# Performance work log

Measured on AMD Instinct MI355X. Metric: run time of the kernel, lower is better.

The kernel has to match this reference:

```python
import jax, jax.numpy as jnp
import numpy as np

DIM = 256
HEADS = 8
H = 32
W = 32
N = H * W  # must equal 4*DIM for the BatchNorm1d(dim*4) over the token dim to be valid
TAU = 2.0
V_TH = 1.0


def _rope_rotations():
    # RoPE buffer: shape (H, W, DIM//2) angles; k_max = DIM // (2*2)
    k_max = DIM // 4
    theta = 1.0 / (10000.0 ** (jnp.arange(k_max, dtype=jnp.float32) / k_max))
    hg, wg = jnp.meshgrid(jnp.arange(H, dtype=jnp.float32), jnp.arange(W, dtype=jnp.float32), indexing='ij')
    angles = jnp.concatenate([hg[..., None] * theta, wg[..., None] * theta], axis=-1)  # (H,W,DIM//2)
    return jnp.cos(angles), jnp.sin(angles)


def _apply_rope(x, cos, sin):
    # x: (b,H,W,DIM); complex rotation on consecutive (re,im) pairs
    x2 = x.reshape(*x.shape[:-1], -1, 2)
    re, im = x2[..., 0], x2[..., 1]
    out = jnp.stack([cos * re - sin * im, sin * re + cos * im], axis=-1)
    return out.reshape(x.shape)


def _lif(x):
    # MultiStepLIFNode(tau=2.0, detach_reset=True): time axis = axis 0 (here batch, as in source),
    # decay_input=True, v_reset=0 (hard reset), heaviside fwd + sigmoid(alpha=4) surrogate bwd.
    def step(v, xt):
        v = v + (xt - v) / TAU
        sg = jax.nn.sigmoid(4.0 * (v - V_TH))
        spike = jax.lax.stop_gradient((v >= V_TH).astype(x.dtype) - sg) + sg
        v = v * (1.0 - jax.lax.stop_gradient(spike))  # detach_reset hard reset to 0
        return v, spike
    _, s = jax.lax.scan(step, jnp.zeros_like(x[0]), x)
    return s


def setup_inputs() -> dict:
    key = jax.random.key(0)
    ks = jax.random.split(key, 4)
    x = jax.random.normal(ks[0], (8, N, DIM), dtype=jnp.float32)
    Wqk = jax.random.normal(ks[1], (DIM, 2 * DIM), dtype=jnp.float32) * 0.02
    bqk = jnp.zeros((2 * DIM,), dtype=jnp.float32)
    bn_gamma = jnp.ones((N,), dtype=jnp.float32)
    bn_beta = jnp.zeros((N,), dtype=jnp.float32)
    lepe_w = jax.random.normal(ks[2], (DIM, 1, 3, 3), dtype=jnp.float32) * 0.1
    lepe_b = jnp.zeros((DIM,), dtype=jnp.float32)
    return {"x": x, "Wqk": Wqk, "bqk": bqk, "bn_gamma": bn_gamma, "bn_beta": bn_beta,
            "lepe_w": lepe_w, "lepe_b": lepe_b}


def reference(x, Wqk, bqk, bn_gamma, bn_beta, lepe_w, lepe_b):
    b, n, c = x.shape
    hd = c // HEADS
    cos, sin = _rope_rotations()

    qk = x @ Wqk + bqk  # (b,n,2c)
    # Dropout is identity in eval. BatchNorm1d(4*dim) in eval mode: channels = token dim (n == 4*dim),
    # running_mean=0, running_var=1 -> pure affine per token index.
    qk = qk * bn_gamma[None, :, None] + bn_beta[None, :, None]
    qk = _lif(qk)
    q, k = qk[..., :c], qk[..., c:]  # reshape(b,n,2,c) split
    v = x
    q = jax.nn.elu(q) + 1.0
    k = jax.nn.elu(k) + 1.0

    q_rope = _apply_rope(q.reshape(b, H, W, c), cos, sin).reshape(b, n, HEADS, hd).transpose(0, 2, 1, 3)
    k_rope = _apply_rope(k.reshape(b, H, W, c), cos, sin).reshape(b, n, HEADS, hd).transpose(0, 2, 1, 3)
    qh = q.reshape(b, n, HEADS, hd).transpose(0, 2, 1, 3)  # (b,h,n,d)
    kh = k.reshape(b, n, HEADS, hd).transpose(0, 2, 1, 3)
    vh = v.reshape(b, n, HEADS, hd).transpose(0, 2, 1, 3)

    atten = jnp.einsum('bhnd,bhmd->bhnm', qh, kh)  # returned, not used for output
    kmean = kh.mean(axis=2, keepdims=True)  # (b,h,1,d)
    z = 1.0 / (jnp.einsum('bhnd,bhed->bhne', qh, kmean) + 1e-6)  # (b,h,n,1)
    kv = jnp.einsum('bhnd,bhne->bhde', k_rope, vh) / n  # (k^T n^-0.5) @ (v n^-0.5)
    out = jnp.einsum('bhnd,bhde->bhne', q_rope, kv) * z  # (b,h,n,d)
    out = out.transpose(0, 2, 1, 3).reshape(b, n, c)

    v_img = vh.transpose(0, 2, 1, 3).reshape(b, H, W, c).transpose(0, 3, 1, 2)  # (b,c,H,W)
    lepe = jax.lax.conv_general_dilated(v_img, lepe_w, (1, 1), 'SAME',
                                        feature_group_count=c,
                                        dimension_numbers=('NCHW', 'OIHW', 'NCHW'))
    lepe = lepe + lepe_b[None, :, None, None]
    out = out + lepe.transpose(0, 2, 3, 1).reshape(b, n, c)
    return (out, qh, kh, v_img, atten)
```

## Files before the change

### kernel.cpp

```cpp
#include <hip/hip_runtime.h>
#include <cstdint>
#include <cstddef>

#define OFF_OUT   0
#define OFF_QH    2097152
#define OFF_KH    4194304
#define OFF_VIMG  6291456
#define OFF_ATT   8388608

#define WS_MQ   0
#define WS_MK   65536
#define WS_TBL  131072
#define WS_KVP  393216
#define WS_KMP  655360

typedef float f32x4 __attribute__((ext_vector_type(4)));

__device__ __forceinline__ void gemm_lif_512(
    const float* __restrict__ x, const float* __restrict__ Wqk,
    const float* __restrict__ bqk, const float* __restrict__ gamma,
    const float* __restrict__ beta, unsigned* __restrict__ mq,
    unsigned* __restrict__ mk, float* smem, unsigned* nib,
    int blk_n, int blk_c, int t)
{
    int ks = t >> 8, tl = t & 255;
    int n0 = blk_n * 8, c0 = blk_c * 128;
    int c_t = tl & 31, n_l = tl >> 5;
    float* xs  = smem + ks * 2176;
    float* wsb = smem + 4352 + ks * 4224;

    float acc[8][4];
    #pragma unroll
    for (int b = 0; b < 8; ++b)
        #pragma unroll
        for (int j = 0; j < 4; ++j) acc[b][j] = 0.f;

    int um = tl >> 3, ukq = tl & 7;
    const float* gx1 = x + ((size_t)(um & 7) * 1024 + n0 + (um >> 3)) * 256 + ks * 128 + ukq * 4;
    const float* gx2 = gx1 + 4 * 256;
    float* lx1 = xs + (ukq * 4) * 68 + um;
    float* lx2 = lx1 + 32;
    const float* gw = Wqk + ((size_t)ks * 128 + (tl >> 5)) * 512 + c0 + (tl & 31) * 4;
    float* lw0 = wsb + (tl >> 5) * 132 + (tl & 31) * 4;

    f32x4 px0, px1, pw0, pw1, pw2, pw3;
    px0 = *(const f32x4*)(gx1);
    px1 = *(const f32x4*)(gx2);
    pw0 = *(const f32x4*)(gw);
    pw1 = *(const f32x4*)(gw + 8 * 512);
    pw2 = *(const f32x4*)(gw + 16 * 512);
    pw3 = *(const f32x4*)(gw + 24 * 512);

    for (int p = 0; p < 4; ++p) {
        #pragma unroll
        for (int j = 0; j < 4; ++j) { lx1[j * 68] = px0[j]; lx2[j * 68] = px1[j]; }
        *(f32x4*)(lw0)            = pw0;
        *(f32x4*)(lw0 + 8 * 132)  = pw1;
        *(f32x4*)(lw0 + 16 * 132) = pw2;
        *(f32x4*)(lw0 + 24 * 132) = pw3;
        __syncthreads();
        if (p < 3) {
            int ko = (p + 1) * 32;
            px0 = *(const f32x4*)(gx1 + ko);
            px1 = *(const f32x4*)(gx2 + ko);
            pw0 = *(const f32x4*)(gw + (ko + 0) * 512);
            pw1 = *(const f32x4*)(gw + (ko + 8) * 512);
            pw2 = *(const f32x4*)(gw + (ko + 16) * 512);
            pw3 = *(const f32x4*)(gw + (ko + 24) * 512);
        }
        #pragma unroll 8
        for (int kk = 0; kk < 32; ++kk) {
            f32x4 xa  = *(const f32x4*)(xs + kk * 68 + n_l * 8);
            f32x4 xb2 = *(const f32x4*)(xs + kk * 68 + n_l * 8 + 4);
            f32x4 w4  = *(const f32x4*)(wsb + kk * 132 + c_t * 4);
            #pragma unroll
            for (int b = 0; b < 4; ++b)
                #pragma unroll
                for (int j = 0; j < 4; ++j)
                    acc[b][j] = fmaf(xa[b], w4[j], acc[b][j]);
            #pragma unroll
            for (int b = 0; b < 4; ++b)
                #pragma unroll
                for (int j = 0; j < 4; ++j)
                    acc[b + 4][j] = fmaf(xb2[b], w4[j], acc[b + 4][j]);
        }
        __syncthreads();
    }

    float* comb = smem;
    if (ks == 1) {
        #pragma unroll
        for (int idx = 0; idx < 32; ++idx)
            comb[idx * 257 + tl] = acc[idx >> 2][idx & 3];
    }
    __syncthreads();
    if (ks == 0) {
        #pragma unroll
        for (int idx = 0; idx < 32; ++idx)
            acc[idx >> 2][idx & 3] += comb[idx * 257 + tl];
        float g = gamma[n0 + n_l], be = beta[n0 + n_l];
        f32x4 bq = *(const f32x4*)&bqk[c0 + c_t * 4];
        float v0 = 0.f, v1 = 0.f, v2 = 0.f, v3 = 0.f;
        #pragma unroll
        for (int b = 0; b < 8; ++b) {
            float a0 = (acc[b][0] + bq[0]) * g + be;
            float a1 = (acc[b][1] + bq[1]) * g + be;
            float a2 = (acc[b][2] + bq[2]) * g + be;
            float a3 = (acc[b][3] + bq[3]) * g + be;
            v0 = v0 + (a0 - v0) * 0.5f; v1 = v1 + (a1 - v1) * 0.5f;
            v2 = v2 + (a2 - v2) * 0.5f; v3 = v3 + (a3 - v3) * 0.5f;
            unsigned s0 = (v0 >= 1.f), s1 = (v1 >= 1.f), s2 = (v2 >= 1.f), s3 = (v3 >= 1.f);
            v0 = s0 ? 0.f : v0; v1 = s1 ? 0.f : v1;
            v2 = s2 ? 0.f : v2; v3 = s3 ? 0.f : v3;
            nib[n_l * 256 + (c_t >> 3) * 64 + (c_t & 7) * 8 + b] =
                s0 | (s1 << 1) | (s2 << 2) | (s3 << 3);
        }
    }
    __syncthreads();
    if (t < 256) {
        int b = t & 7, hp = (t >> 3) & 3, nl = t >> 5;
        unsigned wd = 0;
        #pragma unroll
        for (int c8 = 0; c8 < 8; ++c8)
            wd |= nib[nl * 256 + hp * 64 + c8 * 8 + b] << (4 * c8);
        unsigned h = (unsigned)((blk_c & 1) * 4 + hp);
        unsigned* dst = (blk_c < 2) ? mq : mk;
        dst[b * 8192 + h * 1024 + n0 + nl] = wd;
    }
}

__global__ __launch_bounds__(512) void phaseA_kernel(
    const float* __restrict__ x, const float* __restrict__ Wqk,
    const float* __restrict__ bqk, const float* __restrict__ gamma,
    const float* __restrict__ beta, unsigned* __restrict__ mq,
    unsigned* __restrict__ mk, float* __restrict__ vimg,
    float* __restrict__ tbl)
{
    __shared__ float smem[12800];
    __shared__ unsigned nib[2048];
    int t = threadIdx.x;
    int blk = blockIdx.x;
    if (blk < 256) {
        gemm_lif_512(x, Wqk, bqk, gamma, beta, mq, mk, smem, nib,
                     blk >> 1, 2 + (blk & 1), t);
        return;
    }
    if (blk >= 1280) {
        int id = (blk - 1280) * 512 + t;
        int j = id & 127, n = id >> 7;
        int i = (j < 64) ? j : j - 64;
        float th = powf(10000.0f, -(float)i * (1.0f / 64.0f));
        float pos = (float)((j < 64) ? (n >> 5) : (n & 31));
        float ang = pos * th;
        tbl[n * 256 + j * 2]     = cosf(ang);
        tbl[n * 256 + j * 2 + 1] = sinf(ang);
        return;
    }
    int tile = (blk - 256) * 2 + (t >> 8);
    int st = t & 255;
    float* s = smem + (t >> 8) * 1056;
    int b = tile >> 8, ti = tile & 255;
    int p0 = (ti >> 3) * 32, c0 = (ti & 7) * 32;
    int row = st >> 3, c4 = (st & 7) * 4;
    const float4 vl = *(const float4*)&x[(b * 1024 + p0 + row) * 256 + c0 + c4];
    s[row * 33 + c4 + 0] = vl.x; s[row * 33 + c4 + 1] = vl.y;
    s[row * 33 + c4 + 2] = vl.z; s[row * 33 + c4 + 3] = vl.w;
    __syncthreads();
    int cc = st >> 3, p4 = (st & 7) * 4;
    f32x4 o;
    o.x = s[(p4 + 0) * 33 + cc]; o.y = s[(p4 + 1) * 33 + cc];
    o.z = s[(p4 + 2) * 33 + cc]; o.w = s[(p4 + 3) * 33 + cc];
    *(f32x4*)&vimg[(b * 256 + c0 + cc) * 1024 + p0 + p4] = o;
}

__global__ __launch_bounds__(512) void phaseB_kernel(
    const float* __restrict__ x, const float* __restrict__ Wqk,
    const float* __restrict__ bqk, const float* __restrict__ gamma,
    const float* __restrict__ beta, unsigned* __restrict__ mq,
    unsigned* __restrict__ mk, const float* __restrict__ tbl,
    float* __restrict__ kvp, float* __restrict__ kmp)
{
    __shared__ float smem[12800];
    __shared__ unsigned nib[2048];
    int t = threadIdx.x;
    int blk = blockIdx.x;
    if (blk < 256) {
        gemm_lif_512(x, Wqk, bqk, gamma, beta, mq, mk, smem, nib,
                     blk >> 1, blk & 1, t);
        return;
    }
    int ks2 = t >> 8, tl = t & 255;
    int unit = (blk - 256) * 2 + ks2;
    int bh = unit >> 2, seg = unit & 3;
    int b = bh >> 3, h = bh & 7;
    int n0 = seg * 256;
    float* kr   = smem + ks2 * 4800;
    float* vhs  = kr + 2304;
    float* part = kr + 4416;
    int d = tl & 31, ch = tl >> 5;
    int sc = 0;
    for (int i = 0; i < 32; ++i)
        sc += (mk[bh * 1024 + n0 + ch * 32 + i] >> d) & 1u;
    part[ch * 32 + d] = (float)sc;
    __syncthreads();
    if (tl < 32) {
        float cs = 0.f;
        #pragma unroll
        for (int j = 0; j < 8; ++j) cs += part[j * 32 + tl];
        kmp[bh * 128 + seg * 32 + tl] = cs;
    }
    float a0 = 0, a1 = 0, a2 = 0, a3 = 0;
    int e = tl & 31, db = (tl >> 5) * 4;
    for (int c0 = n0; c0 < n0 + 256; c0 += 64) {
        __syncthreads();
        #pragma unroll
        for (int i = 0; i < 8; ++i) {
            int f = tl + i * 256;
            int nn = f >> 5, dd = f & 31;
            int n = c0 + nn;
            unsigned w = mk[bh * 1024 + n];
            float kd = 1.0f + (float)((w >> dd) & 1u);
            float ko = 1.0f + (float)((w >> (dd ^ 1)) & 1u);
            const float* cp = tbl + n * 256 + h * 32 + (dd & ~1);
            float cc2 = cp[0], ss2 = cp[1];
            kr[nn * 36 + dd] = (dd & 1) ? (ss2 * ko + cc2 * kd) : (cc2 * kd - ss2 * ko);
            vhs[nn * 33 + dd] = x[(b * 1024 + n) * 256 + h * 32 + dd];
        }
        __syncthreads();
        #pragma unroll 8
        for (int nn = 0; nn < 64; ++nn) {
            float ve = vhs[nn * 33 + e];
            float4 kk = *(const float4*)&kr[nn * 36 + db];
            a0 = fmaf(kk.x, ve, a0); a1 = fmaf(kk.y, ve, a1);
            a2 = fmaf(kk.z, ve, a2); a3 = fmaf(kk.w, ve, a3);
        }
    }
    float* dst = kvp + bh * 4096 + seg * 1024;
    dst[(db + 0) * 32 + e] = a0;
    dst[(db + 1) * 32 + e] = a1;
    dst[(db + 2) * 32 + e] = a2;
    dst[(db + 3) * 32 + e] = a3;
}

__global__ __launch_bounds__(256) void phaseC_kernel(
    const unsigned* __restrict__ mq, const unsigned* __restrict__ mk,
    const float* __restrict__ x, const float* __restrict__ tbl,
    const float* __restrict__ kvp, const float* __restrict__ kmp,
    const float* __restrict__ lw, const float* __restrict__ lb,
    float* __restrict__ outbase)
{
    int t = threadIdx.x;
    if (blockIdx.x >= 512) {
        int blk = blockIdx.x - 512;
        int bh = blk >> 5;
        int tile = blk & 31;
        float* qh = outbase + OFF_QH;
        float* kh = outbase + OFF_KH;
        float* att = outbase + OFF_ATT;
        {
            int row = tile * 32 + (t >> 3);
            int d0 = (t & 7) * 4;
            unsigned wq = mq[bh * 1024 + row], wk = mk[bh * 1024 + row];
            f32x4 a, bb;
            a.x = 1.f + (float)((wq >> (d0 + 0)) & 1u);
            a.y = 1.f + (float)((wq >> (d0 + 1)) & 1u);
            a.z = 1.f + (float)((wq >> (d0 + 2)) & 1u);
            a.w = 1.f + (float)((wq >> (d0 + 3)) & 1u);
            bb.x = 1.f + (float)((wk >> (d0 + 0)) & 1u);
            bb.y = 1.f + (float)((wk >> (d0 + 1)) & 1u);
            bb.z = 1.f + (float)((wk >> (d0 + 2)) & 1u);
            bb.w = 1.f + (float)((wk >> (d0 + 3)) & 1u);
            *(f32x4*)&qh[((bh * 1024 + row) << 5) + d0] = a;
            *(f32x4*)&kh[((bh * 1024 + row) << 5) + d0] = bb;
        }
        uint4 mm = ((const uint4*)(mk + bh * 1024))[t];
        float4 rr;
        rr.x = (float)__popc(mm.x); rr.y = (float)__popc(mm.y);
        rr.z = (float)__popc(mm.z); rr.w = (float)__popc(mm.w);
        float* base = att + ((size_t)bh * 1024 + (size_t)tile * 32) * 1024;
        const unsigned* mqrow = mq + bh * 1024 + tile * 32;
        for (int row = 0; row < 32; ++row) {
            unsigned mqw = mqrow[row];
            float rq = 32.0f + (float)__popc(mqw);
            f32x4 o;
            o.x = rq + rr.x + (float)__popc(mqw & mm.x);
            o.y = rq + rr.y + (float)__popc(mqw & mm.y);
            o.z = rq + rr.z + (float)__popc(mqw & mm.z);
            o.w = rq + rr.w + (float)__popc(mqw & mm.w);
            ((f32x4*)(base + (size_t)row * 1024))[t] = o;
        }
        return;
    }
    int bi = blockIdx.x;
    int bh = bi >> 3, sub = bi & 7;
    int pseg = sub >> 1, half = sub & 1;
    int b = bh >> 3, h = bh & 7;
    bool hy = (h < 4);
    int e = t & 31, p_l = t >> 5;
    int p = pseg * 8 + p_l;
    int q0 = half * 16;
    float* out = outbase + OFF_OUT;

    __shared__ float kvs[32][32];
    __shared__ float kmf[32];
    __shared__ float zs[128];
    const float inv = 1.0f / 1024.0f;
    #pragma unroll
    for (int i = 0; i < 4; ++i) {
        int f = t + i * 256;
        const float* kp = kvp + bh * 4096 + f;
        kvs[f >> 5][f & 31] = (kp[0] + kp[1024] + kp[2048] + kp[3072]) * inv;
    }
    if (t < 32) {
        const float* mp = kmp + bh * 128 + t;
        kmf[t] = 1.0f + (mp[0] + mp[32] + mp[64] + mp[96]) * inv;
    }
    __syncthreads();
    float S = 0.f;
    #pragma unroll
    for (int dd = 0; dd < 32; ++dd) S += kmf[dd];
    if (t < 128) {
        int pl2 = t >> 4, iq = t & 15;
        int pp = pseg * 8 + pl2, qq = q0 + iq;
        int n = hy ? (pp * 32 + qq) : (qq * 32 + pp);
        unsigned w = mq[bh * 1024 + n];
        float acc = S;
        #pragma unroll
        for (int dd = 0; dd < 32; ++dd)
            acc += (float)((w >> dd) & 1u) * kmf[dd];
        zs[t] = 1.0f / (acc + 1e-6f);
    }
    int n_ref = hy ? (p * 32) : p;
    const float* cp = tbl + n_ref * 256 + h * 32;
    float E[16], O[16], B = 0.f;
    #pragma unroll
    for (int j = 0; j < 16; ++j) {
        float c2 = cp[2 * j], s2 = cp[2 * j + 1];
        float K0 = kvs[2 * j][e], K1 = kvs[2 * j + 1][e];
        E[j] = c2 * K0 + s2 * K1;
        O[j] = c2 * K1 - s2 * K0;
        B += E[j] + O[j];
    }
    __syncthreads();
    int c = h * 32 + e;
    float w9[9];
    #pragma unroll
    for (int j = 0; j < 9; ++j) w9[j] = lw[c * 9 + j];
    float lbv = lb[c];
    const float* xb = x + (size_t)b * 262144 + c;
    auto ld = [&](int yy, int xx) -> float {
        if ((unsigned)yy > 31u || (unsigned)xx > 31u) return 0.f;
        return xb[(yy * 32 + xx) * 256];
    };
    if (hy) {
        int y = p;
        float Wm0 = ld(y - 1, q0 - 1), Wm1 = ld(y, q0 - 1), Wm2 = ld(y + 1, q0 - 1);
        float Wc0 = ld(y - 1, q0),     Wc1 = ld(y, q0),     Wc2 = ld(y + 1, q0);
        #pragma unroll 4
        for (int i = 0; i < 16; ++i) {
            int m = q0 + i;
            float Wp0 = ld(y - 1, m + 1), Wp1 = ld(y, m + 1), Wp2 = ld(y + 1, m + 1);
            int n = y * 32 + m;
            unsigned w = mq[bh * 1024 + n];
            float o = B;
            #pragma unroll
            for (int j = 0; j < 16; ++j) {
                o += (float)((w >> (2 * j)) & 1u) * E[j];
                o += (float)((w >> (2 * j + 1)) & 1u) * O[j];
            }
            o *= zs[p_l * 16 + i];
            float l = lbv;
            l = fmaf(w9[0], Wm0, l); l = fmaf(w9[1], Wc0, l); l = fmaf(w9[2], Wp0, l);
            l = fmaf(w9[3], Wm1, l); l = fmaf(w9[4], Wc1, l); l = fmaf(w9[5], Wp1, l);
            l = fmaf(w9[6], Wm2, l); l = fmaf(w9[7], Wc2, l); l = fmaf(w9[8], Wp2, l);
            out[((b * 1024 + n) << 8) + c] = o + l;
            Wm0 = Wc0; Wm1 = Wc1; Wm2 = Wc2;
            Wc0 = Wp0; Wc1 = Wp1; Wc2 = Wp2;
        }
    } else {
        int xx0 = p;
        float Wm0 = ld(q0 - 1, xx0 - 1), Wm1 = ld(q0 - 1, xx0), Wm2 = ld(q0 - 1, xx0 + 1);
        float Wc0 = ld(q0, xx0 - 1),     Wc1 = ld(q0, xx0),     Wc2 = ld(q0, xx0 + 1);
        #pragma unroll 4
        for (int i = 0; i < 16; ++i) {
            int m = q0 + i;
            float Wp0 = ld(m + 1, xx0 - 1), Wp1 = ld(m + 1, xx0), Wp2 = ld(m + 1, xx0 + 1);
            int n = m * 32 + xx0;
            unsigned w = mq[bh * 1024 + n];
            float o = B;
            #pragma unroll
            for (int j = 0; j < 16; ++j) {
                o += (float)((w >> (2 * j)) & 1u) * E[j];
                o += (float)((w >> (2 * j + 1)) & 1u) * O[j];
            }
            o *= zs[p_l * 16 + i];
            float l = lbv;
            l = fmaf(w9[0], Wm0, l); l = fmaf(w9[1], Wm1, l); l = fmaf(w9[2], Wm2, l);
            l = fmaf(w9[3], Wc0, l); l = fmaf(w9[4], Wc1, l); l = fmaf(w9[5], Wc2, l);
            l = fmaf(w9[6], Wp0, l); l = fmaf(w9[7], Wp1, l); l = fmaf(w9[8], Wp2, l);
            out[((b * 1024 + n) << 8) + c] = o + l;
            Wm0 = Wc0; Wm1 = Wc1; Wm2 = Wc2;
            Wc0 = Wp0; Wc1 = Wp1; Wc2 = Wp2;
        }
    }
}

extern "C" void kernel_launch(void* const* d_in, const int* in_sizes, int n_in,
                              void* d_out, int out_size, void* d_ws, size_t ws_size,
                              hipStream_t stream)
{
    const float* x     = (const float*)d_in[0];
    const float* Wqk   = (const float*)d_in[1];
    const float* bqk   = (const float*)d_in[2];
    const float* gamma = (const float*)d_in[3];
    const float* beta  = (const float*)d_in[4];
    const float* lw    = (const float*)d_in[5];
    const float* lb    = (const float*)d_in[6];
    float* out = (float*)d_out;
    unsigned* ws = (unsigned*)d_ws;
    unsigned* mq = ws + WS_MQ;
    unsigned* mk = ws + WS_MK;
    float* tbl  = (float*)(ws + WS_TBL);
    float* kvp  = (float*)(ws + WS_KVP);
    float* kmp  = (float*)(ws + WS_KMP);

    hipLaunchKernelGGL(phaseA_kernel, dim3(1536), dim3(512), 0, stream,
                       x, Wqk, bqk, gamma, beta, mq, mk, out + OFF_VIMG, tbl);
    hipLaunchKernelGGL(phaseB_kernel, dim3(384), dim3(512), 0, stream,
                       x, Wqk, bqk, gamma, beta, mq, mk, tbl, kvp, kmp);
    hipLaunchKernelGGL(phaseC_kernel, dim3(2560), dim3(256), 0, stream,
                       mq, mk, x, tbl, kvp, kmp, lw, lb, out);
}
```

Measured before the change: 95.35 us.

## Restructure QK GEMM+LIF tile: per-wave token rows, double buffering, ballot spike packing

Rewrites the fused QK projection + LIF block so each wave owns one token row across all 8 timesteps and each lane computes two channels, replacing the split-K over two 256-thread halves and its shared-memory reduction. Weight and x tiles are double-buffered in LDS with one barrier per K step. Spike bits are packed with wave ballots and bit-spreading instead of going through a nibble scratch array and a second pass. This drops the cross-half reduction and extra syncs, at the cost of less register blocking per thread (16 accumulators instead of 32), which lowers FMA-to-load intensity.

```diff
diff --git a/kernel.cpp b/kernel.cpp
--- a/kernel.cpp
+++ b/kernel.cpp
@@ -16,116 +16,100 @@
 
 typedef float f32x4 __attribute__((ext_vector_type(4)));
 
+__device__ __forceinline__ unsigned spread2(unsigned v) {
+    v = (v | (v << 8)) & 0x00FF00FFu;
+    v = (v | (v << 4)) & 0x0F0F0F0Fu;
+    v = (v | (v << 2)) & 0x33333333u;
+    v = (v | (v << 1)) & 0x55555555u;
+    return v;
+}
+
 __device__ __forceinline__ void gemm_lif_512(
     const float* __restrict__ x, const float* __restrict__ Wqk,
     const float* __restrict__ bqk, const float* __restrict__ gamma,
     const float* __restrict__ beta, unsigned* __restrict__ mq,
-    unsigned* __restrict__ mk, float* smem, unsigned* nib,
+    unsigned* __restrict__ mk, float* pool,
     int blk_n, int blk_c, int t)
 {
-    int ks = t >> 8, tl = t & 255;
-    int n0 = blk_n * 8, c0 = blk_c * 128;
-    int c_t = tl & 31, n_l = tl >> 5;
-    float* xs  = smem + ks * 2176;
-    float* wsb = smem + 4352 + ks * 4224;
-
-    float acc[8][4];
-    #pragma unroll
-    for (int b = 0; b < 8; ++b)
+    const int w = t >> 6, lane = t & 63;
+    const int n0 = blk_n * 8, c0 = blk_c * 128;
+    const int n = n0 + w;
+    const float* gw = Wqk + (size_t)(t >> 5) * 512 + c0 + (t & 31) * 4;
+    const float* gx = x + ((size_t)(lane >> 3) * 1024 + n) * 256 + (lane & 7) * 4;
+    float* wd_base = pool + (t >> 5) * 128 + (t & 31) * 4;
+    float* xs_w    = pool + 8192 + w * 288 + (lane >> 3) * 36 + (lane & 7) * 4;
+    const float* xs_rd = pool + 8192 + w * 288;
+
+    float acc[8][2];
+    #pragma unroll
+    for (int b = 0; b < 8; ++b) { acc[b][0] = 0.f; acc[b][1] = 0.f; }
+
+    {
+        f32x4 wA = *(const f32x4*)(gw);
+        f32x4 wB = *(const f32x4*)(gw + (size_t)16 * 512);
+        f32x4 xr = *(const f32x4*)(gx);
+        *(f32x4*)(wd_base) = wA;
+        *(f32x4*)(wd_base + 2048) = wB;
+        *(f32x4*)(xs_w) = xr;
+    }
+    f32x4 wA_n = *(const f32x4*)(gw + (size_t)32 * 512);
+    f32x4 wB_n = *(const f32x4*)(gw + (size_t)48 * 512);
+    f32x4 xr_n = *(const f32x4*)(gx + 32);
+
+    for (int p = 0; p < 8; ++p) {
+        __syncthreads();
+        if (p < 7) {
+            int nb = (p + 1) & 1;
+            *(f32x4*)(wd_base + nb * 4096)        = wA_n;
+            *(f32x4*)(wd_base + nb * 4096 + 2048) = wB_n;
+            *(f32x4*)(xs_w + nb * 2304)           = xr_n;
+            if (p < 6) {
+                int ko = (p + 2) * 32;
+                wA_n = *(const f32x4*)(gw + (size_t)ko * 512);
+                wB_n = *(const f32x4*)(gw + (size_t)(ko + 16) * 512);
+                xr_n = *(const f32x4*)(gx + ko);
+            }
+        }
+        const float* wsp = pool + (p & 1) * 4096;
+        const float* xsp = xs_rd + (p & 1) * 2304;
         #pragma unroll
-        for (int j = 0; j < 4; ++j) acc[b][j] = 0.f;
-
-    int um = tl >> 3, ukq = tl & 7;
-    const float* gx1 = x + ((size_t)(um & 7) * 1024 + n0 + (um >> 3)) * 256 + ks * 128 + ukq * 4;
-    const float* gx2 = gx1 + 4 * 256;
-    float* lx1 = xs + (ukq * 4) * 68 + um;
-    float* lx2 = lx1 + 32;
-    const float* gw = Wqk + ((size_t)ks * 128 + (tl >> 5)) * 512 + c0 + (tl & 31) * 4;
-    float* lw0 = wsb + (tl >> 5) * 132 + (tl & 31) * 4;
-
-    f32x4 px0, px1, pw0, pw1, pw2, pw3;
-    px0 = *(const f32x4*)(gx1);
-    px1 = *(const f32x4*)(gx2);
-    pw0 = *(const f32x4*)(gw);
-    pw1 = *(const f32x4*)(gw + 8 * 512);
-    pw2 = *(const f32x4*)(gw + 16 * 512);
-    pw3 = *(const f32x4*)(gw + 24 * 512);
-
-    for (int p = 0; p < 4; ++p) {
-        #pragma unroll
-        for (int j = 0; j < 4; ++j) { lx1[j * 68] = px0[j]; lx2[j * 68] = px1[j]; }
-        *(f32x4*)(lw0)            = pw0;
-        *(f32x4*)(lw0 + 8 * 132)  = pw1;
-        *(f32x4*)(lw0 + 16 * 132) = pw2;
-        *(f32x4*)(lw0 + 24 * 132) = pw3;
-        __syncthreads();
-        if (p < 3) {
-            int ko = (p + 1) * 32;
-            px0 = *(const f32x4*)(gx1 + ko);
-            px1 = *(const f32x4*)(gx2 + ko);
-            pw0 = *(const f32x4*)(gw + (ko + 0) * 512);
-            pw1 = *(const f32x4*)(gw + (ko + 8) * 512);
-            pw2 = *(const f32x4*)(gw + (ko + 16) * 512);
-            pw3 = *(const f32x4*)(gw + (ko + 24) * 512);
-        }
-        #pragma unroll 8
-        for (int kk = 0; kk < 32; ++kk) {
-            f32x4 xa  = *(const f32x4*)(xs + kk * 68 + n_l * 8);
-            f32x4 xb2 = *(const f32x4*)(xs + kk * 68 + n_l * 8 + 4);
-            f32x4 w4  = *(const f32x4*)(wsb + kk * 132 + c_t * 4);
+        for (int kk4 = 0; kk4 < 8; ++kk4) {
+            f32x4 xv[8];
             #pragma unroll
-            for (int b = 0; b < 4; ++b)
+            for (int b = 0; b < 8; ++b)
+                xv[b] = *(const f32x4*)(xsp + b * 36 + kk4 * 4);
+            #pragma unroll
+            for (int j = 0; j < 4; ++j) {
+                float2 w2 = *(const float2*)(wsp + (kk4 * 4 + j) * 128 + lane * 2);
                 #pragma unroll
-                for (int j = 0; j < 4; ++j)
-                    acc[b][j] = fmaf(xa[b], w4[j], acc[b][j]);
-            #pragma unroll
-            for (int b = 0; b < 4; ++b)
-                #pragma unroll
-                for (int j = 0; j < 4; ++j)
-                    acc[b + 4][j] = fmaf(xb2[b], w4[j], acc[b + 4][j]);
-        }
-        __syncthreads();
-    }
-
-    float* comb = smem;
-    if (ks == 1) {
-        #pragma unroll
-        for (int idx = 0; idx < 32; ++idx)
-            comb[idx * 257 + tl] = acc[idx >> 2][idx & 3];
-    }
-    __syncthreads();
-    if (ks == 0) {
-        #pragma unroll
-        for (int idx = 0; idx < 32; ++idx)
-            acc[idx >> 2][idx & 3] += comb[idx * 257 + tl];
-        float g = gamma[n0 + n_l], be = beta[n0 + n_l];
-        f32x4 bq = *(const f32x4*)&bqk[c0 + c_t * 4];
-        float v0 = 0.f, v1 = 0.f, v2 = 0.f, v3 = 0.f;
-        #pragma unroll
-        for (int b = 0; b < 8; ++b) {
-            float a0 = (acc[b][0] + bq[0]) * g + be;
-            float a1 = (acc[b][1] + bq[1]) * g + be;
-            float a2 = (acc[b][2] + bq[2]) * g + be;
-            float a3 = (acc[b][3] + bq[3]) * g + be;
-            v0 = v0 + (a0 - v0) * 0.5f; v1 = v1 + (a1 - v1) * 0.5f;
-            v2 = v2 + (a2 - v2) * 0.5f; v3 = v3 + (a3 - v3) * 0.5f;
-            unsigned s0 = (v0 >= 1.f), s1 = (v1 >= 1.f), s2 = (v2 >= 1.f), s3 = (v3 >= 1.f);
-            v0 = s0 ? 0.f : v0; v1 = s1 ? 0.f : v1;
-            v2 = s2 ? 0.f : v2; v3 = s3 ? 0.f : v3;
-            nib[n_l * 256 + (c_t >> 3) * 64 + (c_t & 7) * 8 + b] =
-                s0 | (s1 << 1) | (s2 << 2) | (s3 << 3);
-        }
-    }
-    __syncthreads();
-    if (t < 256) {
-        int b = t & 7, hp = (t >> 3) & 3, nl = t >> 5;
-        unsigned wd = 0;
-        #pragma unroll
-        for (int c8 = 0; c8 < 8; ++c8)
-            wd |= nib[nl * 256 + hp * 64 + c8 * 8 + b] << (4 * c8);
-        unsigned h = (unsigned)((blk_c & 1) * 4 + hp);
-        unsigned* dst = (blk_c < 2) ? mq : mk;
-        dst[b * 8192 + h * 1024 + n0 + nl] = wd;
+                for (int b = 0; b < 8; ++b) {
+                    acc[b][0] = fmaf(xv[b][j], w2.x, acc[b][0]);
+                    acc[b][1] = fmaf(xv[b][j], w2.y, acc[b][1]);
+                }
+            }
+        }
+    }
+
+    float g = gamma[n], be = beta[n];
+    float2 bq = *(const float2*)&bqk[c0 + lane * 2];
+    unsigned* dst = (blk_c < 2) ? mq : mk;
+    int hbase = (blk_c & 1) * 4;
+    float v0 = 0.f, v1 = 0.f;
+    #pragma unroll
+    for (int b = 0; b < 8; ++b) {
+        float a0 = (acc[b][0] + bq.x) * g + be;
+        float a1 = (acc[b][1] + bq.y) * g + be;
+        v0 = v0 + (a0 - v0) * 0.5f;
+        v1 = v1 + (a1 - v1) * 0.5f;
+        bool s0 = (v0 >= 1.f), s1 = (v1 >= 1.f);
+        v0 = s0 ? 0.f : v0; v1 = s1 ? 0.f : v1;
+        unsigned long long m0 = __ballot(s0 ? 1 : 0);
+        unsigned long long m1 = __ballot(s1 ? 1 : 0);
+        if (lane < 4) {
+            unsigned a = (unsigned)(m0 >> (lane * 16)) & 0xFFFFu;
+            unsigned c = (unsigned)(m1 >> (lane * 16)) & 0xFFFFu;
+            dst[b * 8192 + (hbase + lane) * 1024 + n] = spread2(a) | (spread2(c) << 1);
+        }
     }
 }
 
@@ -137,11 +121,10 @@
     float* __restrict__ tbl)
 {
     __shared__ float smem[12800];
-    __shared__ unsigned nib[2048];
     int t = threadIdx.x;
     int blk = blockIdx.x;
     if (blk < 256) {
-        gemm_lif_512(x, Wqk, bqk, gamma, beta, mq, mk, smem, nib,
+        gemm_lif_512(x, Wqk, bqk, gamma, beta, mq, mk, smem,
                      blk >> 1, 2 + (blk & 1), t);
         return;
     }
@@ -181,11 +164,10 @@
     float* __restrict__ kvp, float* __restrict__ kmp)
 {
     __shared__ float smem[12800];
-    __shared__ unsigned nib[2048];
     int t = threadIdx.x;
     int blk = blockIdx.x;
     if (blk < 256) {
-        gemm_lif_512(x, Wqk, bqk, gamma, beta, mq, mk, smem, nib,
+        gemm_lif_512(x, Wqk, bqk, gamma, beta, mq, mk, smem,
                      blk >> 1, blk & 1, t);
         return;
     }
```

Measured after the change: 160.1 us. 1.68x slower.

## Shrink GEMM-LIF blocks to 256 threads with 8x8 register tiles

Applied to the files above, without the earlier changes.

The fused QK GEMM plus LIF routine now runs with 256 threads per block instead of 512, and each thread computes an 8x8 accumulator tile instead of 8x4. The W shared-memory layout is padded and interleaved to reduce bank conflicts, and spike bits are packed as bytes rather than nibbles. The auxiliary transpose, RoPE-table and kv-partial work in phases A and B is also re-split to one unit per 256-thread block. The aim is more register-level reuse per shared-memory load and finer-grained blocks, at the cost of higher register pressure and fewer threads per GEMM tile.

```diff
diff --git a/kernel.cpp b/kernel.cpp
--- a/kernel.cpp
+++ b/kernel.cpp
@@ -16,137 +16,149 @@
 
 typedef float f32x4 __attribute__((ext_vector_type(4)));
 
-__device__ __forceinline__ void gemm_lif_512(
+__device__ __forceinline__ int wcol(int g) { return g * 8 + 4 * (g >> 2); }
+
+__device__ __forceinline__ void gemm_lif_256(
     const float* __restrict__ x, const float* __restrict__ Wqk,
     const float* __restrict__ bqk, const float* __restrict__ gamma,
     const float* __restrict__ beta, unsigned* __restrict__ mq,
-    unsigned* __restrict__ mk, float* smem, unsigned* nib,
+    unsigned* __restrict__ mk, float* pool,
     int blk_n, int blk_c, int t)
 {
-    int ks = t >> 8, tl = t & 255;
-    int n0 = blk_n * 8, c0 = blk_c * 128;
-    int c_t = tl & 31, n_l = tl >> 5;
-    float* xs  = smem + ks * 2176;
-    float* wsb = smem + 4352 + ks * 4224;
-
-    float acc[8][4];
+    const int ks = t >> 7, tl = t & 127;
+    const int c_t = tl & 15, n_l = tl >> 4;
+    const int n0 = blk_n * 8, c0 = blk_c * 128;
+    float* wpool = pool + ks * 4480;
+    float* xpool = pool + 8960 + ks * 2176;
+
+    float acc[8][8];
     #pragma unroll
     for (int b = 0; b < 8; ++b)
         #pragma unroll
-        for (int j = 0; j < 4; ++j) acc[b][j] = 0.f;
-
-    int um = tl >> 3, ukq = tl & 7;
-    const float* gx1 = x + ((size_t)(um & 7) * 1024 + n0 + (um >> 3)) * 256 + ks * 128 + ukq * 4;
-    const float* gx2 = gx1 + 4 * 256;
-    float* lx1 = xs + (ukq * 4) * 68 + um;
-    float* lx2 = lx1 + 32;
-    const float* gw = Wqk + ((size_t)ks * 128 + (tl >> 5)) * 512 + c0 + (tl & 31) * 4;
-    float* lw0 = wsb + (tl >> 5) * 132 + (tl & 31) * 4;
-
-    f32x4 px0, px1, pw0, pw1, pw2, pw3;
-    px0 = *(const f32x4*)(gx1);
-    px1 = *(const f32x4*)(gx2);
-    pw0 = *(const f32x4*)(gw);
-    pw1 = *(const f32x4*)(gw + 8 * 512);
-    pw2 = *(const f32x4*)(gw + 16 * 512);
-    pw3 = *(const f32x4*)(gw + 24 * 512);
+        for (int j = 0; j < 8; ++j) acc[b][j] = 0.f;
+
+    const int um = tl >> 3, ukq = tl & 7;
+    const float* gx0 = x + ((size_t)(um & 7) * 1024 + n0 + (um >> 3)) * 256
+                         + ks * 128 + ukq * 4;
+    const float* gw0 = Wqk + (size_t)(ks * 128 + (tl >> 5)) * 512 + c0 + (tl & 31) * 4;
+    const int wg = (tl & 31) >> 1;
+    float* lw_ = wpool + (tl >> 5) * 140 + wcol(wg) + (tl & 1) * 4;
+    float* lx_ = xpool + (ukq * 4) * 68 + um;
+
+    f32x4 px[4], pw[8];
+    #pragma unroll
+    for (int i = 0; i < 4; ++i) px[i] = *(const f32x4*)(gx0 + (size_t)(i * 2) * 256);
+    #pragma unroll
+    for (int i = 0; i < 8; ++i) pw[i] = *(const f32x4*)(gw0 + (size_t)(i * 4) * 512);
 
     for (int p = 0; p < 4; ++p) {
         #pragma unroll
-        for (int j = 0; j < 4; ++j) { lx1[j * 68] = px0[j]; lx2[j * 68] = px1[j]; }
-        *(f32x4*)(lw0)            = pw0;
-        *(f32x4*)(lw0 + 8 * 132)  = pw1;
-        *(f32x4*)(lw0 + 16 * 132) = pw2;
-        *(f32x4*)(lw0 + 24 * 132) = pw3;
+        for (int i = 0; i < 4; ++i)
+            #pragma unroll
+            for (int j = 0; j < 4; ++j)
+                lx_[j * 68 + i * 16] = px[i][j];
+        #pragma unroll
+        for (int i = 0; i < 8; ++i)
+            *(f32x4*)(lw_ + i * 4 * 140) = pw[i];
         __syncthreads();
         if (p < 3) {
             int ko = (p + 1) * 32;
-            px0 = *(const f32x4*)(gx1 + ko);
-            px1 = *(const f32x4*)(gx2 + ko);
-            pw0 = *(const f32x4*)(gw + (ko + 0) * 512);
-            pw1 = *(const f32x4*)(gw + (ko + 8) * 512);
-            pw2 = *(const f32x4*)(gw + (ko + 16) * 512);
-            pw3 = *(const f32x4*)(gw + (ko + 24) * 512);
-        }
+            #pragma unroll
+            for (int i = 0; i < 4; ++i)
+                px[i] = *(const f32x4*)(gx0 + (size_t)(i * 2) * 256 + ko);
+            #pragma unroll
+            for (int i = 0; i < 8; ++i)
+                pw[i] = *(const f32x4*)(gw0 + (size_t)(ko + i * 4) * 512);
+        }
+        const int xc = n_l * 8;
+        const int wc = wcol(c_t);
         #pragma unroll 8
         for (int kk = 0; kk < 32; ++kk) {
-            f32x4 xa  = *(const f32x4*)(xs + kk * 68 + n_l * 8);
-            f32x4 xb2 = *(const f32x4*)(xs + kk * 68 + n_l * 8 + 4);
-            f32x4 w4  = *(const f32x4*)(wsb + kk * 132 + c_t * 4);
-            #pragma unroll
-            for (int b = 0; b < 4; ++b)
+            f32x4 xa = *(const f32x4*)(xpool + kk * 68 + xc);
+            f32x4 xb = *(const f32x4*)(xpool + kk * 68 + xc + 4);
+            f32x4 wa = *(const f32x4*)(wpool + kk * 140 + wc);
+            f32x4 wb = *(const f32x4*)(wpool + kk * 140 + wc + 4);
+            #pragma unroll
+            for (int b = 0; b < 4; ++b) {
                 #pragma unroll
-                for (int j = 0; j < 4; ++j)
-                    acc[b][j] = fmaf(xa[b], w4[j], acc[b][j]);
-            #pragma unroll
-            for (int b = 0; b < 4; ++b)
-                #pragma unroll
-                for (int j = 0; j < 4; ++j)
-                    acc[b + 4][j] = fmaf(xb2[b], w4[j], acc[b + 4][j]);
+                for (int j = 0; j < 4; ++j) {
+                    acc[b][j]         = fmaf(xa[b], wa[j], acc[b][j]);
+                    acc[b][j + 4]     = fmaf(xa[b], wb[j], acc[b][j + 4]);
+                    acc[b + 4][j]     = fmaf(xb[b], wa[j], acc[b + 4][j]);
+                    acc[b + 4][j + 4] = fmaf(xb[b], wb[j], acc[b + 4][j + 4]);
+                }
+            }
         }
         __syncthreads();
     }
 
-    float* comb = smem;
+    float* comb = pool;
     if (ks == 1) {
         #pragma unroll
-        for (int idx = 0; idx < 32; ++idx)
-            comb[idx * 257 + tl] = acc[idx >> 2][idx & 3];
-    }
-    __syncthreads();
+        for (int b = 0; b < 8; ++b)
+            #pragma unroll
+            for (int j = 0; j < 8; ++j)
+                comb[(b * 8 + j) * 129 + tl] = acc[b][j];
+    }
+    __syncthreads();
+    unsigned char* nib = (unsigned char*)(pool + 8960);
     if (ks == 0) {
         #pragma unroll
-        for (int idx = 0; idx < 32; ++idx)
-            acc[idx >> 2][idx & 3] += comb[idx * 257 + tl];
+        for (int b = 0; b < 8; ++b)
+            #pragma unroll
+            for (int j = 0; j < 8; ++j)
+                acc[b][j] += comb[(b * 8 + j) * 129 + tl];
         float g = gamma[n0 + n_l], be = beta[n0 + n_l];
-        f32x4 bq = *(const f32x4*)&bqk[c0 + c_t * 4];
-        float v0 = 0.f, v1 = 0.f, v2 = 0.f, v3 = 0.f;
+        f32x4 bqa = *(const f32x4*)(bqk + c0 + c_t * 8);
+        f32x4 bqb = *(const f32x4*)(bqk + c0 + c_t * 8 + 4);
+        float v[8];
+        #pragma unroll
+        for (int j = 0; j < 8; ++j) v[j] = 0.f;
         #pragma unroll
         for (int b = 0; b < 8; ++b) {
-            float a0 = (acc[b][0] + bq[0]) * g + be;
-            float a1 = (acc[b][1] + bq[1]) * g + be;
-            float a2 = (acc[b][2] + bq[2]) * g + be;
-            float a3 = (acc[b][3] + bq[3]) * g + be;
-            v0 = v0 + (a0 - v0) * 0.5f; v1 = v1 + (a1 - v1) * 0.5f;
-            v2 = v2 + (a2 - v2) * 0.5f; v3 = v3 + (a3 - v3) * 0.5f;
-            unsigned s0 = (v0 >= 1.f), s1 = (v1 >= 1.f), s2 = (v2 >= 1.f), s3 = (v3 >= 1.f);
-            v0 = s0 ? 0.f : v0; v1 = s1 ? 0.f : v1;
-            v2 = s2 ? 0.f : v2; v3 = s3 ? 0.f : v3;
-            nib[n_l * 256 + (c_t >> 3) * 64 + (c_t & 7) * 8 + b] =
-                s0 | (s1 << 1) | (s2 << 2) | (s3 << 3);
-        }
-    }
-    __syncthreads();
-    if (t < 256) {
-        int b = t & 7, hp = (t >> 3) & 3, nl = t >> 5;
+            unsigned byte = 0;
+            #pragma unroll
+            for (int j = 0; j < 8; ++j) {
+                float bqv = (j < 4) ? bqa[j] : bqb[j - 4];
+                float a = (acc[b][j] + bqv) * g + be;
+                v[j] = v[j] + (a - v[j]) * 0.5f;
+                bool sp = (v[j] >= 1.f);
+                v[j] = sp ? 0.f : v[j];
+                byte |= (sp ? 1u : 0u) << j;
+            }
+            nib[n_l * 128 + c_t * 8 + b] = (unsigned char)byte;
+        }
+    }
+    __syncthreads();
+    {
+        int b = t & 7, w = (t >> 3) & 3, nl = t >> 5;
         unsigned wd = 0;
         #pragma unroll
-        for (int c8 = 0; c8 < 8; ++c8)
-            wd |= nib[nl * 256 + hp * 64 + c8 * 8 + b] << (4 * c8);
-        unsigned h = (unsigned)((blk_c & 1) * 4 + hp);
+        for (int j = 0; j < 4; ++j)
+            wd |= (unsigned)nib[nl * 128 + (w * 4 + j) * 8 + b] << (8 * j);
+        unsigned h = (unsigned)((blk_c & 1) * 4 + w);
         unsigned* dst = (blk_c < 2) ? mq : mk;
         dst[b * 8192 + h * 1024 + n0 + nl] = wd;
     }
 }
 
-__global__ __launch_bounds__(512) void phaseA_kernel(
+__global__ __launch_bounds__(256) void phaseA_kernel(
     const float* __restrict__ x, const float* __restrict__ Wqk,
     const float* __restrict__ bqk, const float* __restrict__ gamma,
     const float* __restrict__ beta, unsigned* __restrict__ mq,
     unsigned* __restrict__ mk, float* __restrict__ vimg,
     float* __restrict__ tbl)
 {
-    __shared__ float smem[12800];
-    __shared__ unsigned nib[2048];
+    __shared__ float smem[13312];
     int t = threadIdx.x;
     int blk = blockIdx.x;
     if (blk < 256) {
-        gemm_lif_512(x, Wqk, bqk, gamma, beta, mq, mk, smem, nib,
+        gemm_lif_256(x, Wqk, bqk, gamma, beta, mq, mk, smem,
                      blk >> 1, 2 + (blk & 1), t);
         return;
     }
-    if (blk >= 1280) {
-        int id = (blk - 1280) * 512 + t;
+    if (blk >= 2304) {
+        int id = (blk - 2304) * 256 + t;
         int j = id & 127, n = id >> 7;
         int i = (j < 64) ? j : j - 64;
         float th = powf(10000.0f, -(float)i * (1.0f / 64.0f));
@@ -156,66 +168,63 @@
         tbl[n * 256 + j * 2 + 1] = sinf(ang);
         return;
     }
-    int tile = (blk - 256) * 2 + (t >> 8);
-    int st = t & 255;
-    float* s = smem + (t >> 8) * 1056;
+    float* s = smem;
+    int tile = blk - 256;
     int b = tile >> 8, ti = tile & 255;
     int p0 = (ti >> 3) * 32, c0 = (ti & 7) * 32;
-    int row = st >> 3, c4 = (st & 7) * 4;
+    int row = t >> 3, c4 = (t & 7) * 4;
     const float4 vl = *(const float4*)&x[(b * 1024 + p0 + row) * 256 + c0 + c4];
     s[row * 33 + c4 + 0] = vl.x; s[row * 33 + c4 + 1] = vl.y;
     s[row * 33 + c4 + 2] = vl.z; s[row * 33 + c4 + 3] = vl.w;
     __syncthreads();
-    int cc = st >> 3, p4 = (st & 7) * 4;
+    int cc = t >> 3, p4 = (t & 7) * 4;
     f32x4 o;
     o.x = s[(p4 + 0) * 33 + cc]; o.y = s[(p4 + 1) * 33 + cc];
     o.z = s[(p4 + 2) * 33 + cc]; o.w = s[(p4 + 3) * 33 + cc];
     *(f32x4*)&vimg[(b * 256 + c0 + cc) * 1024 + p0 + p4] = o;
 }
 
-__global__ __launch_bounds__(512) void phaseB_kernel(
+__global__ __launch_bounds__(256) void phaseB_kernel(
     const float* __restrict__ x, const float* __restrict__ Wqk,
     const float* __restrict__ bqk, const float* __restrict__ gamma,
     const float* __restrict__ beta, unsigned* __restrict__ mq,
     unsigned* __restrict__ mk, const float* __restrict__ tbl,
     float* __restrict__ kvp, float* __restrict__ kmp)
 {
-    __shared__ float smem[12800];
-    __shared__ unsigned nib[2048];
+    __shared__ float smem[13312];
     int t = threadIdx.x;
     int blk = blockIdx.x;
     if (blk < 256) {
-        gemm_lif_512(x, Wqk, bqk, gamma, beta, mq, mk, smem, nib,
+        gemm_lif_256(x, Wqk, bqk, gamma, beta, mq, mk, smem,
                      blk >> 1, blk & 1, t);
         return;
     }
-    int ks2 = t >> 8, tl = t & 255;
-    int unit = (blk - 256) * 2 + ks2;
+    int unit = blk - 256;
     int bh = unit >> 2, seg = unit & 3;
     int b = bh >> 3, h = bh & 7;
     int n0 = seg * 256;
-    float* kr   = smem + ks2 * 4800;
-    float* vhs  = kr + 2304;
-    float* part = kr + 4416;
-    int d = tl & 31, ch = tl >> 5;
+    float* kr   = smem;
+    float* vhs  = smem + 2304;
+    float* part = smem + 4416;
+    int d = t & 31, ch = t >> 5;
     int sc = 0;
     for (int i = 0; i < 32; ++i)
         sc += (mk[bh * 1024 + n0 + ch * 32 + i] >> d) & 1u;
     part[ch * 32 + d] = (float)sc;
     __syncthreads();
-    if (tl < 32) {
+    if (t < 32) {
         float cs = 0.f;
         #pragma unroll
-        for (int j = 0; j < 8; ++j) cs += part[j * 32 + tl];
-        kmp[bh * 128 + seg * 32 + tl] = cs;
+        for (int j = 0; j < 8; ++j) cs += part[j * 32 + t];
+        kmp[bh * 128 + seg * 32 + t] = cs;
     }
     float a0 = 0, a1 = 0, a2 = 0, a3 = 0;
-    int e = tl & 31, db = (tl >> 5) * 4;
+    int e = t & 31, db = (t >> 5) * 4;
     for (int c0 = n0; c0 < n0 + 256; c0 += 64) {
         __syncthreads();
         #pragma unroll
         for (int i = 0; i < 8; ++i) {
-            int f = tl + i * 256;
+            int f = t + i * 256;
             int nn = f >> 5, dd = f & 31;
             int n = c0 + nn;
             unsigned w = mk[bh * 1024 + n];
@@ -424,9 +433,9 @@
     float* kvp  = (float*)(ws + WS_KVP);
     float* kmp  = (float*)(ws + WS_KMP);
 
-    hipLaunchKernelGGL(phaseA_kernel, dim3(1536), dim3(512), 0, stream,
+    hipLaunchKernelGGL(phaseA_kernel, dim3(2816), dim3(256), 0, stream,
                        x, Wqk, bqk, gamma, beta, mq, mk, out + OFF_VIMG, tbl);
-    hipLaunchKernelGGL(phaseB_kernel, dim3(384), dim3(512), 0, stream,
+    hipLaunchKernelGGL(phaseB_kernel, dim3(512), dim3(256), 0, stream,
                        x, Wqk, bqk, gamma, beta, mq, mk, tbl, kvp, kmp);
     hipLaunchKernelGGL(phaseC_kernel, dim3(2560), dim3(256), 0, stream,
                        mq, mk, x, tbl, kvp, kmp, lw, lb, out);
```

New measurement: 95.30 us, median of 2. About the same (-0.1%).
